# Kernel optimization log

Hardware: AMD Instinct MI355X
Metric: run time of the kernel (lower is better)

The kernel has to match this reference:

```python
import jax, jax.numpy as jnp
import numpy as np

# static architecture constants (match init_kwargs)
H, D, N_BASIS, MEM_LEN, QLEN = 16, 128, 1024, 512, 2048
RIDGE = 0.5
BASIS_SIGMAS = (0.005, 0.01)


def _gaussian_pdf(x, mu, sigma):
    return jnp.exp(-0.5 * ((x - mu) / sigma) ** 2) / (sigma * jnp.sqrt(2.0 * jnp.pi))


def _basis_params(n):
    # torch.meshgrid(linspace(0,1,n//2), sigmas, indexing='ij') then flatten
    m = jnp.linspace(0.0, 1.0, n // len(BASIS_SIGMAS)).astype(jnp.float32)
    mu = jnp.repeat(m, len(BASIS_SIGMAS))
    sigma = jnp.tile(jnp.asarray(BASIS_SIGMAS, jnp.float32), n // len(BASIS_SIGMAS))
    return mu, sigma


def _compute_G(l, b_mu, b_sigma, n):
    # padded linear positions on [-0.5+shift, 1.5-shift], l even -> 2l points
    shift = 1.0 / (2 * l)
    pos = jnp.linspace(-0.5 + shift, 1.5 - shift, 2 * l).astype(jnp.float32)
    F = _gaussian_pdf(pos[None, :], b_mu[:, None], b_sigma[:, None])  # [N, 2l]
    # G = F^T (F F^T + ridge I)^{-1}, then crop padding rows -> [l, N]
    G = jnp.linalg.solve(F @ F.T + RIDGE * jnp.eye(n, dtype=jnp.float32), F).T
    return G[l // 2: -(l // 2)]


def _forward(k, q, W_key, W_val, W_out, w_mu, w_sigma):
    d = H * D
    b_mu, b_sigma = _basis_params(N_BASIS)
    k = k[:, -512:, :]                                   # forward truncates memory
    l = k.shape[1]
    G = _compute_G(l, b_mu, b_sigma, N_BASIS)            # [l, N]
    # value_function: project signal onto basis coefficients B -> [1, N, d]
    B = jnp.einsum('bld,ln->bnd', k, G)
    keys = (B @ W_key.T).reshape(1, N_BASIS, H, D).transpose(0, 2, 1, 3)    # [1,H,N,D]
    values = (B @ W_val.T).reshape(1, N_BASIS, H, D).transpose(0, 2, 1, 3)  # [1,H,N,D]
    scores = jnp.einsum('bhqd,bhnd->bhqn', q / jnp.sqrt(jnp.float32(D)), keys)
    mu = jax.nn.sigmoid(scores @ w_mu)[..., None]                           # [1,H,Q,1]
    sigma_sq = jnp.maximum(jax.nn.softplus(scores @ w_sigma), 1e-4)[..., None]
    # continuous softmax over Gaussian RBFs: r_j = E_{t~N(mu,sigma_sq)}[psi_j(t)]
    # closed form: N(mu; b_mu_j, sigma_sq + b_sigma_j^2)
    r = _gaussian_pdf(b_mu, mu, jnp.sqrt(sigma_sq + b_sigma ** 2))          # [1,H,Q,N]
    context = jnp.einsum('bhqn,bhnd->bqhd', r, values).reshape(1, QLEN, d)
    return context @ W_out.T


def setup_inputs() -> dict:
    key = jax.random.key(0)
    ks = jax.random.split(key, 7)
    d = H * D
    s = 0.02
    return {
        'k': jax.random.normal(ks[0], (1, MEM_LEN, d), jnp.float32),
        'q': jax.random.normal(ks[1], (1, H, QLEN, D), jnp.float32),
        'W_key': jax.random.normal(ks[2], (d, d), jnp.float32) * s,
        'W_val': jax.random.normal(ks[3], (d, d), jnp.float32) * s,
        'W_out': jax.random.normal(ks[4], (d, d), jnp.float32) * s,
        'w_mu': jax.random.normal(ks[5], (N_BASIS,), jnp.float32) * s,
        'w_sigma': jax.random.normal(ks[6], (N_BASIS,), jnp.float32) * s,
        'new_doc': 1,
    }


def reference(k, q, W_key, W_val, W_out, w_mu, w_sigma, new_doc):
    # new_doc=True -> B_past/x_past reset, so only the fresh-memory path runs
    return _forward(k, q, W_key, W_val, W_out, w_mu, w_sigma)
```

## Files before the change

### kernel.cpp

```cpp
#include <hip/hip_runtime.h>
#include <hip/hip_bf16.h>
#include <vector>
#include <cmath>
#include <cstring>

using bf16 = __hip_bfloat16;
typedef short s16x8 __attribute__((ext_vector_type(8)));
typedef float f32x4 __attribute__((ext_vector_type(4)));

static constexpr int kH = 16, kD = 128, kNB = 1024, kML = 512, kQL = 2048, kDM = 2048;

static void compute_Gt_host(float* Gt) {
  const int n = kNB, P = 2 * kML;
  std::vector<double> F((size_t)n * P), A((size_t)n * n), pos(P);
  const double shift = 1.0 / (double)P;
  const double p0 = -0.5 + shift, p1 = 1.5 - shift;
  for (int i = 0; i < P; i++) pos[i] = p0 + (p1 - p0) * (double)i / (double)(P - 1);
  const double c0 = 0.3989422804014327;
  std::vector<int> lo(n), hi(n);
  for (int b = 0; b < n; b++) {
    double mu = (double)(b >> 1) / 511.0;
    double sg = (b & 1) ? 0.01 : 0.005;
    double c = c0 / sg;
    double* Fb = &F[(size_t)b * P];
    for (int i = 0; i < P; i++) { double t = (pos[i] - mu) / sg; Fb[i] = c * exp(-0.5 * t * t); }
    int l = 0; while (l < P - 1 && pos[l] < mu - 14.0 * sg) l++;
    int h = P - 1; while (h > 0 && pos[h] > mu + 14.0 * sg) h--;
    lo[b] = l; hi[b] = h;
  }
  for (int i = 0; i < n; i++) {
    const double* fi = &F[(size_t)i * P];
    for (int j = 0; j <= i; j++) {
      const double* fj = &F[(size_t)j * P];
      int a = lo[i] > lo[j] ? lo[i] : lo[j];
      int b2 = hi[i] < hi[j] ? hi[i] : hi[j];
      double s = 0.0;
      for (int k2 = a; k2 <= b2; k2++) s += fi[k2] * fj[k2];
      A[(size_t)i * n + j] = s;
      if (i != j) A[(size_t)j * n + i] = s;
    }
    A[(size_t)i * n + i] += 0.5;
  }
  for (int j = 0; j < n; j++) {
    double* Aj = &A[(size_t)j * n];
    double d = Aj[j];
    for (int k2 = 0; k2 < j; k2++) d -= Aj[k2] * Aj[k2];
    d = std::sqrt(d); Aj[j] = d;
    double inv = 1.0 / d;
    for (int i = j + 1; i < n; i++) {
      double* Ai = &A[(size_t)i * n];
      double s = Ai[j];
      for (int k2 = 0; k2 < j; k2++) s -= Ai[k2] * Aj[k2];
      Ai[j] = s * inv;
    }
  }
  for (int i = 0; i < n; i++) {
    double* yi = &F[(size_t)i * P];
    const double* Ai = &A[(size_t)i * n];
    for (int k2 = 0; k2 < i; k2++) {
      double lik = Ai[k2];
      const double* yk = &F[(size_t)k2 * P];
      for (int t = 0; t < P; t++) yi[t] -= lik * yk[t];
    }
    double inv = 1.0 / Ai[i];
    for (int t = 0; t < P; t++) yi[t] *= inv;
  }
  for (int i = n - 1; i >= 0; i--) {
    double* xi = &F[(size_t)i * P];
    for (int k2 = i + 1; k2 < n; k2++) {
      double lki = A[(size_t)k2 * n + i];
      const double* xk = &F[(size_t)k2 * P];
      for (int t = 0; t < P; t++) xi[t] -= lki * xk[t];
    }
    double inv = 1.0 / A[(size_t)i * n + i];
    for (int t = 0; t < P; t++) xi[t] *= inv;
  }
  for (int b = 0; b < n; b++)
    for (int l = 0; l < kML; l++)
      Gt[(size_t)b * kML + l] = (float)F[(size_t)b * P + (kML / 2) + l];
}

static unsigned short f2bf_host(float x) {
  unsigned u; std::memcpy(&u, &x, 4);
  unsigned r = (u + 0x7FFFu + ((u >> 16) & 1u)) >> 16;
  return (unsigned short)r;
}
static float bf2f_host(unsigned short b) {
  unsigned u = ((unsigned)b) << 16; float f; std::memcpy(&f, &u, 4); return f;
}

namespace {
struct Init {
  float* d_GtTf = nullptr;
  unsigned short* d_Gth = nullptr;
  unsigned short* d_Gtl = nullptr;
  float* h_GtTf_pinned = nullptr;
  unsigned short* h_Gth_pinned = nullptr;
  unsigned short* h_Gtl_pinned = nullptr;
  std::vector<float> h_GtTf;
  std::vector<unsigned short> h_Gth, h_Gtl;
  Init() {
    std::vector<float> h_Gt((size_t)kNB * kML);
    compute_Gt_host(h_Gt.data());
    h_GtTf.resize(h_Gt.size());
    h_Gth.resize(h_Gt.size());
    h_Gtl.resize(h_Gt.size());
    for (int n = 0; n < kNB; n++)
      for (int l = 0; l < kML; l++) {
        float v = h_Gt[(size_t)n * kML + l];
        h_GtTf[(size_t)l * kNB + n] = v;
        unsigned short hb = f2bf_host(v);
        h_Gth[(size_t)n * kML + l] = hb;
        h_Gtl[(size_t)n * kML + l] = f2bf_host(v - bf2f_host(hb));
      }
    const size_t fb = h_Gt.size() * 4, bb = h_Gt.size() * 2;
    if (hipMalloc((void**)&d_GtTf, fb) == hipSuccess) {
      if (hipMemcpy(d_GtTf, h_GtTf.data(), fb, hipMemcpyHostToDevice) != hipSuccess) { hipFree(d_GtTf); d_GtTf = nullptr; }
    }
    if (hipMalloc((void**)&d_Gth, bb) == hipSuccess) {
      if (hipMemcpy(d_Gth, h_Gth.data(), bb, hipMemcpyHostToDevice) != hipSuccess) { hipFree(d_Gth); d_Gth = nullptr; }
    }
    if (hipMalloc((void**)&d_Gtl, bb) == hipSuccess) {
      if (hipMemcpy(d_Gtl, h_Gtl.data(), bb, hipMemcpyHostToDevice) != hipSuccess) { hipFree(d_Gtl); d_Gtl = nullptr; }
    }
    if (!d_GtTf && hipHostMalloc((void**)&h_GtTf_pinned, fb, 0) == hipSuccess)
      std::memcpy(h_GtTf_pinned, h_GtTf.data(), fb);
    if (!d_Gth && hipHostMalloc((void**)&h_Gth_pinned, bb, 0) == hipSuccess)
      std::memcpy(h_Gth_pinned, h_Gth.data(), bb);
    if (!d_Gtl && hipHostMalloc((void**)&h_Gtl_pinned, bb, 0) == hipSuccess)
      std::memcpy(h_Gtl_pinned, h_Gtl.data(), bb);
  }
};
Init g_init;
}

__device__ inline short f2bf(float x) {
  unsigned u = __float_as_uint(x);
  unsigned r = (u + 0x7FFFu + ((u >> 16) & 1u)) >> 16;
  return (short)r;
}
__device__ inline float bf2f(short b) {
  return __uint_as_float(((unsigned)(unsigned short)b) << 16);
}

__device__ inline void gload16(const void* g, void* l) {
  __builtin_amdgcn_global_load_lds(
      (__attribute__((address_space(1))) void*)(g),
      (__attribute__((address_space(3))) void*)(l),
      16, 0, 0);
}

__global__ __launch_bounds__(256) void detect_kernel(const unsigned short* __restrict__ q,
                                                     int* __restrict__ flag) {
  int t = threadIdx.x;
  int bad = 0;
  for (int i = t; i < 4096; i += 256) {
    int e = (q[i] >> 7) & 0xFF;
    if (e >= 0x98) bad = 1;
  }
  __shared__ int s[256];
  s[t] = bad; __syncthreads();
  for (int k2 = 128; k2 > 0; k2 >>= 1) { if (t < k2) s[t] |= s[t + k2]; __syncthreads(); }
  if (t == 0) *flag = s[0];
}

__global__ __launch_bounds__(256) void conv_bf16(const void* __restrict__ in,
                                                 short* __restrict__ out, int n4,
                                                 const int* __restrict__ flag) {
  int i = blockIdx.x * 256 + threadIdx.x;
  if (i >= n4) return;
  if (*flag) {
    float4 v = ((const float4*)in)[i];
    short4 o; o.x = f2bf(v.x); o.y = f2bf(v.y); o.z = f2bf(v.z); o.w = f2bf(v.w);
    ((short4*)out)[i] = o;
  } else {
    ((short4*)out)[i] = ((const short4*)in)[i];
  }
}

__global__ __launch_bounds__(256) void gw_kernel(const float* __restrict__ GtT,
                                                 const void* __restrict__ wmu,
                                                 const void* __restrict__ wsg,
                                                 float* __restrict__ gw,
                                                 const int* __restrict__ flag) {
  const bool f32 = (*flag != 0);
  const int l = blockIdx.x, t = threadIdx.x;
  const float* row = GtT + (long long)l * kNB;
  float a = 0.f, b = 0.f;
  for (int n = t; n < kNB; n += 256) {
    float g = row[n];
    float wm_ = f32 ? ((const float*)wmu)[n] : bf2f(((const short*)wmu)[n]);
    float ws_ = f32 ? ((const float*)wsg)[n] : bf2f(((const short*)wsg)[n]);
    a += g * wm_; b += g * ws_;
  }
  __shared__ float red[2][256];
  red[0][t] = a; red[1][t] = b;
  __syncthreads();
  for (int s = 128; s > 0; s >>= 1) {
    if (t < s) { red[0][t] += red[0][t + s]; red[1][t] += red[1][t + s]; }
    __syncthreads();
  }
  if (t == 0) { gw[l] = red[0][0]; gw[kML + l] = red[1][0]; }
}

__global__ __launch_bounds__(256) void bwk_kernel(const void* __restrict__ kin,
                                                  const float* __restrict__ gw,
                                                  float* __restrict__ bw,
                                                  const int* __restrict__ flag) {
  const bool f32 = (*flag != 0);
  int j = blockIdx.x * 256 + threadIdx.x;
  int l0 = blockIdx.y * 32;
  float a = 0.f, b = 0.f;
  for (int l = l0; l < l0 + 32; l++) {
    float kv = f32 ? ((const float*)kin)[(long long)l * kDM + j]
                   : bf2f(((const short*)kin)[(long long)l * kDM + j]);
    a += kv * gw[l]; b += kv * gw[kML + l];
  }
  atomicAdd(&bw[j], a);
  atomicAdd(&bw[kDM + j], b);
}

__global__ __launch_bounds__(256) void kw_kernel(const void* __restrict__ Wk,
                                                 const float* __restrict__ bw,
                                                 float* __restrict__ kw,
                                                 const int* __restrict__ flag) {
  const bool f32 = (*flag != 0);
  int i = blockIdx.x;
  float smu = 0.f, ssg = 0.f;
  if (f32) {
    const float* row = (const float*)Wk + (long long)i * kDM;
    for (int j = threadIdx.x; j < kDM; j += 256) { float w = row[j]; smu += w * bw[j]; ssg += w * bw[kDM + j]; }
  } else {
    const short* row = (const short*)Wk + (long long)i * kDM;
    for (int j = threadIdx.x; j < kDM; j += 256) { float w = bf2f(row[j]); smu += w * bw[j]; ssg += w * bw[kDM + j]; }
  }
  __shared__ float red[2][256];
  red[0][threadIdx.x] = smu; red[1][threadIdx.x] = ssg;
  __syncthreads();
  for (int s = 128; s > 0; s >>= 1) {
    if (threadIdx.x < (unsigned)s) {
      red[0][threadIdx.x] += red[0][threadIdx.x + s];
      red[1][threadIdx.x] += red[1][threadIdx.x + s];
    }
    __syncthreads();
  }
  if (threadIdx.x == 0) { kw[i] = red[0][0]; kw[kDM + i] = red[1][0]; }
}

__global__ __launch_bounds__(256) void musig_kernel(const void* __restrict__ q,
                                                    const float* __restrict__ kw,
                                                    float* __restrict__ mu,
                                                    float* __restrict__ sigsq,
                                                    const int* __restrict__ flag) {
  const bool f32 = (*flag != 0);
  int w = threadIdx.x >> 6, lane = threadIdx.x & 63;
  int idx = blockIdx.x * 4 + w;
  int h = idx >> 11;
  const float* kmu = kw + h * kD;
  const float* ksg = kw + kDM + h * kD;
  float q0, q1;
  if (f32) {
    const float* qrow = (const float*)q + (long long)idx * kD;
    q0 = qrow[lane]; q1 = qrow[lane + 64];
  } else {
    const short* qrow = (const short*)q + (long long)idx * kD;
    q0 = bf2f(qrow[lane]); q1 = bf2f(qrow[lane + 64]);
  }
  float a = q0 * kmu[lane] + q1 * kmu[lane + 64];
  float b = q0 * ksg[lane] + q1 * ksg[lane + 64];
  for (int s = 32; s > 0; s >>= 1) { a += __shfl_xor(a, s); b += __shfl_xor(b, s); }
  if (lane == 0) {
    const float inv_sqrt_d = 0.08838834764831845f;
    float zm = a * inv_sqrt_d, zs = b * inv_sqrt_d;
    mu[idx] = 1.f / (1.f + __expf(-zm));
    float sp = (zs > 20.f) ? zs : log1pf(__expf(zs));
    sigsq[idx] = fmaxf(sp, 1e-4f);
  }
}

template <int CSTORE>
__global__ __launch_bounds__(256) void mfma_gemm_bt(
    const short* __restrict__ A0, int lda, long long sA,
    const short* __restrict__ BT0, int ldb, long long sB,
    void* __restrict__ C0, int ldc, long long sC,
    int K, const int* __restrict__ flag) {
  __shared__ s16x8 lA[512];
  __shared__ s16x8 lB[512];
  const short* A = A0 + (long long)blockIdx.z * sA;
  const short* BT = BT0 + (long long)blockIdx.z * sB;
  const int t = threadIdx.x;
  const int wave = t >> 6, lane = t & 63;
  const int quad = lane >> 4, l16 = lane & 15;
  const int wm = wave >> 1, wn = wave & 1;
  const int m0 = blockIdx.y * 128, n0 = blockIdx.x * 128;
  const int srow = lane & 15, skc = lane >> 4;
  f32x4 acc[4][4];
  const f32x4 z = {0.f, 0.f, 0.f, 0.f};
#pragma unroll
  for (int i = 0; i < 4; i++)
#pragma unroll
    for (int j = 0; j < 4; j++) acc[i][j] = z;
  for (int k0 = 0; k0 < K; k0 += 32) {
#pragma unroll
    for (int i = 0; i < 2; i++) {
      int sub = wave + i * 4;
      int m = sub * 16 + srow;
      gload16(A + (long long)(m0 + m) * lda + k0 + skc * 8, &lA[sub * 64]);
      gload16(BT + (long long)(n0 + m) * ldb + k0 + skc * 8, &lB[sub * 64]);
    }
    __syncthreads();
    s16x8 af[4], bfr[4];
#pragma unroll
    for (int i = 0; i < 4; i++) af[i] = lA[(wm * 4 + i) * 64 + lane];
#pragma unroll
    for (int j = 0; j < 4; j++) bfr[j] = lB[(wn * 4 + j) * 64 + lane];
#pragma unroll
    for (int i = 0; i < 4; i++)
#pragma unroll
      for (int j = 0; j < 4; j++)
        acc[i][j] = __builtin_amdgcn_mfma_f32_16x16x32_bf16(af[i], bfr[j], acc[i][j], 0, 0, 0);
    __syncthreads();
  }
  if (CSTORE == 0) {
    short* Cp = (short*)C0 + (long long)blockIdx.z * sC;
#pragma unroll
    for (int i = 0; i < 4; i++)
#pragma unroll
      for (int j = 0; j < 4; j++) {
        int gn = n0 + (wn * 4 + j) * 16 + l16;
#pragma unroll
        for (int rg = 0; rg < 4; rg++) {
          int gm = m0 + (wm * 4 + i) * 16 + quad * 4 + rg;
          Cp[(long long)gm * ldc + gn] = f2bf(acc[i][j][rg]);
        }
      }
  } else {
    if (*flag) {
      float* Cp = (float*)C0 + (long long)blockIdx.z * sC;
#pragma unroll
      for (int i = 0; i < 4; i++)
#pragma unroll
        for (int j = 0; j < 4; j++) {
          int gn = n0 + (wn * 4 + j) * 16 + l16;
#pragma unroll
          for (int rg = 0; rg < 4; rg++) {
            int gm = m0 + (wm * 4 + i) * 16 + quad * 4 + rg;
            Cp[(long long)gm * ldc + gn] = acc[i][j][rg];
          }
        }
    } else {
      short* Cp = (short*)C0 + (long long)blockIdx.z * sC;
#pragma unroll
      for (int i = 0; i < 4; i++)
#pragma unroll
        for (int j = 0; j < 4; j++) {
          int gn = n0 + (wn * 4 + j) * 16 + l16;
#pragma unroll
          for (int rg = 0; rg < 4; rg++) {
            int gm = m0 + (wm * 4 + i) * 16 + quad * 4 + rg;
            Cp[(long long)gm * ldc + gn] = f2bf(acc[i][j][rg]);
          }
        }
    }
  }
}

__global__ __launch_bounds__(256) void mfma_gemm_sk(
    const short* __restrict__ A0, int lda,
    const short* __restrict__ BT0, int ldb,
    float* __restrict__ P, int ldc) {
  __shared__ s16x8 lA[512], lB[512];
  const int t = threadIdx.x;
  const int wave = t >> 6, lane = t & 63;
  const int quad = lane >> 4, l16 = lane & 15;
  const int wm = wave >> 1, wn = wave & 1;
  const int m0 = blockIdx.y * 128, n0 = blockIdx.x * 128;
  const int kbeg = blockIdx.z * 512, kend = kbeg + 512;
  const int srow = lane & 15, skc = lane >> 4;
  f32x4 acc[4][4];
  const f32x4 z = {0.f, 0.f, 0.f, 0.f};
#pragma unroll
  for (int i = 0; i < 4; i++)
#pragma unroll
    for (int j = 0; j < 4; j++) acc[i][j] = z;
  for (int k0 = kbeg; k0 < kend; k0 += 32) {
#pragma unroll
    for (int i = 0; i < 2; i++) {
      int sub = wave + i * 4;
      int m = sub * 16 + srow;
      gload16(A0 + (long long)(m0 + m) * lda + k0 + skc * 8, &lA[sub * 64]);
      gload16(BT0 + (long long)(n0 + m) * ldb + k0 + skc * 8, &lB[sub * 64]);
    }
    __syncthreads();
    s16x8 af[4], bfr[4];
#pragma unroll
    for (int i = 0; i < 4; i++) af[i] = lA[(wm * 4 + i) * 64 + lane];
#pragma unroll
    for (int j = 0; j < 4; j++) bfr[j] = lB[(wn * 4 + j) * 64 + lane];
#pragma unroll
    for (int i = 0; i < 4; i++)
#pragma unroll
      for (int j = 0; j < 4; j++)
        acc[i][j] = __builtin_amdgcn_mfma_f32_16x16x32_bf16(af[i], bfr[j], acc[i][j], 0, 0, 0);
    __syncthreads();
  }
  float* Cp = P + (long long)blockIdx.z * kML * kDM;
#pragma unroll
  for (int i = 0; i < 4; i++)
#pragma unroll
    for (int j = 0; j < 4; j++) {
      int gn = n0 + (wn * 4 + j) * 16 + l16;
#pragma unroll
      for (int rg = 0; rg < 4; rg++) {
        int gm = m0 + (wm * 4 + i) * 16 + quad * 4 + rg;
        Cp[(long long)gm * ldc + gn] = acc[i][j][rg];
      }
    }
}

__global__ __launch_bounds__(256) void reduceT_kernel(const float* __restrict__ P,
                                                      short* __restrict__ kvT) {
  __shared__ float tile[64][65];
  const int bd = blockIdx.x, bl = blockIdx.y;
  const int tx = threadIdx.x & 63, ty = threadIdx.x >> 6;
  for (int i = ty; i < 64; i += 4) {
    int l = bl * 64 + i, d = bd * 64 + tx;
    float s = 0.f;
#pragma unroll
    for (int z = 0; z < 4; z++) s += P[((long long)z * kML + l) * kDM + d];
    tile[i][tx] = s;
  }
  __syncthreads();
  for (int i = ty; i < 64; i += 4) {
    int d = bd * 64 + i, l = bl * 64 + tx;
    kvT[(long long)d * kML + l] = f2bf(tile[tx][i]);
  }
}

__global__ __launch_bounds__(256) void mfma_gemm_bt2(
    const short* __restrict__ A0, int lda,
    const short* __restrict__ BTh, const short* __restrict__ BTl, int ldb,
    short* __restrict__ Ch, short* __restrict__ Cl, int ldc, int K) {
  __shared__ s16x8 lA[512], lBh[512], lBl[512];
  const int t = threadIdx.x;
  const int wave = t >> 6, lane = t & 63;
  const int quad = lane >> 4, l16 = lane & 15;
  const int wm = wave >> 1, wn = wave & 1;
  const int m0 = blockIdx.y * 128, n0 = blockIdx.x * 128;
  const int srow = lane & 15, skc = lane >> 4;
  f32x4 acc[4][4];
  const f32x4 z = {0.f, 0.f, 0.f, 0.f};
#pragma unroll
  for (int i = 0; i < 4; i++)
#pragma unroll
    for (int j = 0; j < 4; j++) acc[i][j] = z;
  for (int k0 = 0; k0 < K; k0 += 32) {
#pragma unroll
    for (int i = 0; i < 2; i++) {
      int sub = wave + i * 4;
      int m = sub * 16 + srow;
      gload16(A0 + (long long)(m0 + m) * lda + k0 + skc * 8, &lA[sub * 64]);
      gload16(BTh + (long long)(n0 + m) * ldb + k0 + skc * 8, &lBh[sub * 64]);
      gload16(BTl + (long long)(n0 + m) * ldb + k0 + skc * 8, &lBl[sub * 64]);
    }
    __syncthreads();
    s16x8 af[4], bh[4], bl[4];
#pragma unroll
    for (int i = 0; i < 4; i++) af[i] = lA[(wm * 4 + i) * 64 + lane];
#pragma unroll
    for (int j = 0; j < 4; j++) {
      bh[j] = lBh[(wn * 4 + j) * 64 + lane];
      bl[j] = lBl[(wn * 4 + j) * 64 + lane];
    }
#pragma unroll
    for (int i = 0; i < 4; i++)
#pragma unroll
      for (int j = 0; j < 4; j++) {
        acc[i][j] = __builtin_amdgcn_mfma_f32_16x16x32_bf16(af[i], bh[j], acc[i][j], 0, 0, 0);
        acc[i][j] = __builtin_amdgcn_mfma_f32_16x16x32_bf16(af[i], bl[j], acc[i][j], 0, 0, 0);
      }
    __syncthreads();
  }
#pragma unroll
  for (int i = 0; i < 4; i++)
#pragma unroll
    for (int j = 0; j < 4; j++) {
      int gn = n0 + (wn * 4 + j) * 16 + l16;
#pragma unroll
      for (int rg = 0; rg < 4; rg++) {
        int gm = m0 + (wm * 4 + i) * 16 + quad * 4 + rg;
        float v = acc[i][j][rg];
        short hb = f2bf(v);
        Ch[(long long)gm * ldc + gn] = hb;
        Cl[(long long)gm * ldc + gn] = f2bf(v - bf2f(hb));
      }
    }
}

__global__ __launch_bounds__(256) void mfma_rv(
    const float* __restrict__ mu_all, const float* __restrict__ s2_all,
    const short* __restrict__ VTh, const short* __restrict__ VTl,
    short* __restrict__ ctx) {
  __shared__ s16x8 lAh[512], lAl[512], lBh[512], lBl[512];
  const int t = threadIdx.x;
  const int wave = t >> 6, lane = t & 63;
  const int quad = lane >> 4, l16 = lane & 15;
  const int wm = wave >> 1, wn = wave & 1;
  const int h = blockIdx.z;
  const int m0 = blockIdx.y * 128;
  const int r0 = t >> 2, kc = t & 3;
  const int srow = lane & 15, skc = lane >> 4;
  const long long voff = (long long)h * kD * kNB;
  float muv[2], ivs[2][2], cof[2][2];
#pragma unroll
  for (int i = 0; i < 2; i++) {
    int row = h * kQL + m0 + r0 + i * 64;
    float m_ = mu_all[row], s2 = s2_all[row];
    ivs[i][0] = rsqrtf(s2 + 2.5e-5f);
    ivs[i][1] = rsqrtf(s2 + 1e-4f);
    cof[i][0] = 0.3989422804014327f * ivs[i][0];
    cof[i][1] = 0.3989422804014327f * ivs[i][1];
    muv[i] = m_;
  }
  f32x4 acc[4][4];
  const f32x4 z = {0.f, 0.f, 0.f, 0.f};
#pragma unroll
  for (int i = 0; i < 4; i++)
#pragma unroll
    for (int j = 0; j < 4; j++) acc[i][j] = z;
  for (int k0 = 0; k0 < kNB; k0 += 32) {
#pragma unroll
    for (int i = 0; i < 2; i++) {
      int sub = wave + i * 4;
      int m = sub * 16 + srow;
      gload16(VTh + voff + (long long)m * kNB + k0 + skc * 8, &lBh[sub * 64]);
      gload16(VTl + voff + (long long)m * kNB + k0 + skc * 8, &lBl[sub * 64]);
    }
#pragma unroll
    for (int i = 0; i < 2; i++) {
      int m = r0 + i * 64;
      int cidx = (m >> 4) * 64 + kc * 16 + (m & 15);
      s16x8 hv, lv;
#pragma unroll
      for (int jj = 0; jj < 8; jj++) {
        int n = k0 + kc * 8 + jj;
        float bmu = (float)(n >> 1) * (1.f / 511.f);
        int p = jj & 1;
        float tt = (bmu - muv[i]) * ivs[i][p];
        float v = cof[i][p] * __expf(-0.5f * tt * tt);
        short hb = f2bf(v);
        hv[jj] = hb;
        lv[jj] = f2bf(v - bf2f(hb));
      }
      lAh[cidx] = hv;
      lAl[cidx] = lv;
    }
    __syncthreads();
    s16x8 ah[4], al[4], bh[4], bl[4];
#pragma unroll
    for (int i = 0; i < 4; i++) {
      ah[i] = lAh[(wm * 4 + i) * 64 + lane];
      al[i] = lAl[(wm * 4 + i) * 64 + lane];
    }
#pragma unroll
    for (int j = 0; j < 4; j++) {
      bh[j] = lBh[(wn * 4 + j) * 64 + lane];
      bl[j] = lBl[(wn * 4 + j) * 64 + lane];
    }
#pragma unroll
    for (int i = 0; i < 4; i++)
#pragma unroll
      for (int j = 0; j < 4; j++) {
        acc[i][j] = __builtin_amdgcn_mfma_f32_16x16x32_bf16(ah[i], bh[j], acc[i][j], 0, 0, 0);
        acc[i][j] = __builtin_amdgcn_mfma_f32_16x16x32_bf16(ah[i], bl[j], acc[i][j], 0, 0, 0);
        acc[i][j] = __builtin_amdgcn_mfma_f32_16x16x32_bf16(al[i], bh[j], acc[i][j], 0, 0, 0);
      }
    __syncthreads();
  }
  short* Cp = ctx + h * kD;
#pragma unroll
  for (int i = 0; i < 4; i++)
#pragma unroll
    for (int j = 0; j < 4; j++) {
      int gn = (wn * 4 + j) * 16 + l16;
#pragma unroll
      for (int rg = 0; rg < 4; rg++) {
        int gm = m0 + (wm * 4 + i) * 16 + quad * 4 + rg;
        Cp[(long long)gm * kDM + gn] = f2bf(acc[i][j][rg]);
      }
    }
}

extern "C" void kernel_launch(void* const* d_in, const int* in_sizes, int n_in,
                              void* d_out, int out_size, void* d_ws, size_t ws_size,
                              hipStream_t stream) {
  (void)in_sizes; (void)n_in; (void)out_size; (void)ws_size;
  const void* kmem = d_in[0];
  const void* q    = d_in[1];
  const void* Wk   = d_in[2];
  const void* Wv   = d_in[3];
  const void* Wo   = d_in[4];
  const void* wmu  = d_in[5];
  const void* wsg  = d_in[6];

  char* ws = (char*)d_ws;
  short* k_bf  = (short*)ws;
  short* kvT   = (short*)(ws + ((size_t)2 << 20));
  short* Wv_bf = (short*)(ws + ((size_t)4 << 20));
  short* Wo_bf = Wv_bf;
  float* Pbuf  = (float*)(ws + ((size_t)12 << 20));
  short* VTh   = (short*)(ws + ((size_t)12 << 20));
  short* VTl   = (short*)(ws + ((size_t)16 << 20));
  short* ctx   = (short*)(ws + ((size_t)20 << 20));
  float* tail  = (float*)(ws + ((size_t)28 << 20));
  float* gw    = tail;
  float* bw    = gw + 2 * kML;
  float* kw    = bw + 2 * kDM;
  float* mu    = kw + 2 * kDM;
  float* sigsq = mu + kH * kQL;
  int*   flag  = (int*)(sigsq + kH * kQL);
  float* gtffall = (float*)(ws + ((size_t)28 << 20) + ((size_t)1 << 19));
  short* ghfall  = (short*)(ws + ((size_t)30 << 20) + ((size_t)1 << 19));
  short* glfall  = (short*)(ws + ((size_t)31 << 20) + ((size_t)1 << 19));

  const float* GtTf = g_init.d_GtTf;
  if (!GtTf) {
    const void* src = g_init.h_GtTf_pinned ? (const void*)g_init.h_GtTf_pinned
                                           : (const void*)g_init.h_GtTf.data();
    hipMemcpyAsync(gtffall, src, (size_t)kNB * kML * 4, hipMemcpyHostToDevice, stream);
    GtTf = gtffall;
  }
  const short* Gh = (const short*)g_init.d_Gth;
  if (!Gh) {
    const void* src = g_init.h_Gth_pinned ? (const void*)g_init.h_Gth_pinned
                                          : (const void*)g_init.h_Gth.data();
    hipMemcpyAsync(ghfall, src, (size_t)kNB * kML * 2, hipMemcpyHostToDevice, stream);
    Gh = ghfall;
  }
  const short* Gl = (const short*)g_init.d_Gtl;
  if (!Gl) {
    const void* src = g_init.h_Gtl_pinned ? (const void*)g_init.h_Gtl_pinned
                                          : (const void*)g_init.h_Gtl.data();
    hipMemcpyAsync(glfall, src, (size_t)kNB * kML * 2, hipMemcpyHostToDevice, stream);
    Gl = glfall;
  }

  detect_kernel<<<1, 256, 0, stream>>>((const unsigned short*)q, flag);

  conv_bf16<<<(kML * kDM / 4 + 255) / 256, 256, 0, stream>>>(kmem, k_bf, kML * kDM / 4, flag);
  conv_bf16<<<(kDM * kDM / 4 + 255) / 256, 256, 0, stream>>>(Wv, Wv_bf, kDM * kDM / 4, flag);

  gw_kernel<<<kML, 256, 0, stream>>>(GtTf, wmu, wsg, gw, flag);
  hipMemsetAsync(bw, 0, 2 * kDM * sizeof(float), stream);
  bwk_kernel<<<dim3(kDM / 256, kML / 32), 256, 0, stream>>>(kmem, gw, bw, flag);
  kw_kernel<<<kDM, 256, 0, stream>>>(Wk, bw, kw, flag);
  musig_kernel<<<kH * kQL / 4, 256, 0, stream>>>(q, kw, mu, sigsq, flag);

  mfma_gemm_sk<<<dim3(kDM / 128, kML / 128, 4), 256, 0, stream>>>(
      k_bf, kDM, Wv_bf, kDM, Pbuf, kDM);
  reduceT_kernel<<<dim3(kDM / 64, kML / 64), 256, 0, stream>>>(Pbuf, kvT);

  conv_bf16<<<(kDM * kDM / 4 + 255) / 256, 256, 0, stream>>>(Wo, Wo_bf, kDM * kDM / 4, flag);

  mfma_gemm_bt2<<<dim3(kNB / 128, kDM / 128, 1), 256, 0, stream>>>(
      kvT, kML, Gh, Gl, kML, VTh, VTl, kNB, kML);

  mfma_rv<<<dim3(1, kQL / 128, kH), 256, 0, stream>>>(mu, sigsq, VTh, VTl, ctx);

  mfma_gemm_bt<2><<<dim3(kDM / 128, kQL / 128, 1), 256, 0, stream>>>(
      ctx, kDM, 0, Wo_bf, kDM, 0, d_out, kDM, 0, kDM, flag);
}
```

Before: 308.2 us.

## Double-buffer LDS tiles in all MFMA GEMM kernels to overlap loads with compute

```diff
diff --git a/kernel.cpp b/kernel.cpp
--- a/kernel.cpp
+++ b/kernel.cpp
@@ -284,8 +284,8 @@
     const short* __restrict__ BT0, int ldb, long long sB,
     void* __restrict__ C0, int ldc, long long sC,
     int K, const int* __restrict__ flag) {
-  __shared__ s16x8 lA[512];
-  __shared__ s16x8 lB[512];
+  __shared__ s16x8 lA[2][512];
+  __shared__ s16x8 lB[2][512];
   const short* A = A0 + (long long)blockIdx.z * sA;
   const short* BT = BT0 + (long long)blockIdx.z * sB;
   const int t = threadIdx.x;
@@ -300,26 +300,38 @@
   for (int i = 0; i < 4; i++)
 #pragma unroll
     for (int j = 0; j < 4; j++) acc[i][j] = z;
+#pragma unroll
+  for (int i = 0; i < 2; i++) {
+    int sub = wave + i * 4;
+    int m = sub * 16 + srow;
+    gload16(A + (long long)(m0 + m) * lda + skc * 8, &lA[0][sub * 64]);
+    gload16(BT + (long long)(n0 + m) * ldb + skc * 8, &lB[0][sub * 64]);
+  }
+  __syncthreads();
+  int cur = 0;
   for (int k0 = 0; k0 < K; k0 += 32) {
-#pragma unroll
-    for (int i = 0; i < 2; i++) {
-      int sub = wave + i * 4;
-      int m = sub * 16 + srow;
-      gload16(A + (long long)(m0 + m) * lda + k0 + skc * 8, &lA[sub * 64]);
-      gload16(BT + (long long)(n0 + m) * ldb + k0 + skc * 8, &lB[sub * 64]);
-    }
-    __syncthreads();
+    if (k0 + 32 < K) {
+      int nxt = cur ^ 1, kk = k0 + 32;
+#pragma unroll
+      for (int i = 0; i < 2; i++) {
+        int sub = wave + i * 4;
+        int m = sub * 16 + srow;
+        gload16(A + (long long)(m0 + m) * lda + kk + skc * 8, &lA[nxt][sub * 64]);
+        gload16(BT + (long long)(n0 + m) * ldb + kk + skc * 8, &lB[nxt][sub * 64]);
+      }
+    }
     s16x8 af[4], bfr[4];
 #pragma unroll
-    for (int i = 0; i < 4; i++) af[i] = lA[(wm * 4 + i) * 64 + lane];
-#pragma unroll
-    for (int j = 0; j < 4; j++) bfr[j] = lB[(wn * 4 + j) * 64 + lane];
+    for (int i = 0; i < 4; i++) af[i] = lA[cur][(wm * 4 + i) * 64 + lane];
+#pragma unroll
+    for (int j = 0; j < 4; j++) bfr[j] = lB[cur][(wn * 4 + j) * 64 + lane];
 #pragma unroll
     for (int i = 0; i < 4; i++)
 #pragma unroll
       for (int j = 0; j < 4; j++)
         acc[i][j] = __builtin_amdgcn_mfma_f32_16x16x32_bf16(af[i], bfr[j], acc[i][j], 0, 0, 0);
     __syncthreads();
+    cur ^= 1;
   }
   if (CSTORE == 0) {
     short* Cp = (short*)C0 + (long long)blockIdx.z * sC;
@@ -369,7 +381,7 @@
     const short* __restrict__ A0, int lda,
     const short* __restrict__ BT0, int ldb,
     float* __restrict__ P, int ldc) {
-  __shared__ s16x8 lA[512], lB[512];
+  __shared__ s16x8 lA[2][512], lB[2][512];
   const int t = threadIdx.x;
   const int wave = t >> 6, lane = t & 63;
   const int quad = lane >> 4, l16 = lane & 15;
@@ -383,26 +395,38 @@
   for (int i = 0; i < 4; i++)
 #pragma unroll
     for (int j = 0; j < 4; j++) acc[i][j] = z;
+#pragma unroll
+  for (int i = 0; i < 2; i++) {
+    int sub = wave + i * 4;
+    int m = sub * 16 + srow;
+    gload16(A0 + (long long)(m0 + m) * lda + kbeg + skc * 8, &lA[0][sub * 64]);
+    gload16(BT0 + (long long)(n0 + m) * ldb + kbeg + skc * 8, &lB[0][sub * 64]);
+  }
+  __syncthreads();
+  int cur = 0;
   for (int k0 = kbeg; k0 < kend; k0 += 32) {
-#pragma unroll
-    for (int i = 0; i < 2; i++) {
-      int sub = wave + i * 4;
-      int m = sub * 16 + srow;
-      gload16(A0 + (long long)(m0 + m) * lda + k0 + skc * 8, &lA[sub * 64]);
-      gload16(BT0 + (long long)(n0 + m) * ldb + k0 + skc * 8, &lB[sub * 64]);
-    }
-    __syncthreads();
+    if (k0 + 32 < kend) {
+      int nxt = cur ^ 1, kk = k0 + 32;
+#pragma unroll
+      for (int i = 0; i < 2; i++) {
+        int sub = wave + i * 4;
+        int m = sub * 16 + srow;
+        gload16(A0 + (long long)(m0 + m) * lda + kk + skc * 8, &lA[nxt][sub * 64]);
+        gload16(BT0 + (long long)(n0 + m) * ldb + kk + skc * 8, &lB[nxt][sub * 64]);
+      }
+    }
     s16x8 af[4], bfr[4];
 #pragma unroll
-    for (int i = 0; i < 4; i++) af[i] = lA[(wm * 4 + i) * 64 + lane];
-#pragma unroll
-    for (int j = 0; j < 4; j++) bfr[j] = lB[(wn * 4 + j) * 64 + lane];
+    for (int i = 0; i < 4; i++) af[i] = lA[cur][(wm * 4 + i) * 64 + lane];
+#pragma unroll
+    for (int j = 0; j < 4; j++) bfr[j] = lB[cur][(wn * 4 + j) * 64 + lane];
 #pragma unroll
     for (int i = 0; i < 4; i++)
 #pragma unroll
       for (int j = 0; j < 4; j++)
         acc[i][j] = __builtin_amdgcn_mfma_f32_16x16x32_bf16(af[i], bfr[j], acc[i][j], 0, 0, 0);
     __syncthreads();
+    cur ^= 1;
   }
   float* Cp = P + (long long)blockIdx.z * kML * kDM;
 #pragma unroll
@@ -441,7 +465,7 @@
     const short* __restrict__ A0, int lda,
     const short* __restrict__ BTh, const short* __restrict__ BTl, int ldb,
     short* __restrict__ Ch, short* __restrict__ Cl, int ldc, int K) {
-  __shared__ s16x8 lA[512], lBh[512], lBl[512];
+  __shared__ s16x8 lA[2][512], lBh[2][512], lBl[2][512];
   const int t = threadIdx.x;
   const int wave = t >> 6, lane = t & 63;
   const int quad = lane >> 4, l16 = lane & 15;
@@ -454,23 +478,35 @@
   for (int i = 0; i < 4; i++)
 #pragma unroll
     for (int j = 0; j < 4; j++) acc[i][j] = z;
+#pragma unroll
+  for (int i = 0; i < 2; i++) {
+    int sub = wave + i * 4;
+    int m = sub * 16 + srow;
+    gload16(A0 + (long long)(m0 + m) * lda + skc * 8, &lA[0][sub * 64]);
+    gload16(BTh + (long long)(n0 + m) * ldb + skc * 8, &lBh[0][sub * 64]);
+    gload16(BTl + (long long)(n0 + m) * ldb + skc * 8, &lBl[0][sub * 64]);
+  }
+  __syncthreads();
+  int cur = 0;
   for (int k0 = 0; k0 < K; k0 += 32) {
-#pragma unroll
-    for (int i = 0; i < 2; i++) {
-      int sub = wave + i * 4;
-      int m = sub * 16 + srow;
-      gload16(A0 + (long long)(m0 + m) * lda + k0 + skc * 8, &lA[sub * 64]);
-      gload16(BTh + (long long)(n0 + m) * ldb + k0 + skc * 8, &lBh[sub * 64]);
-      gload16(BTl + (long long)(n0 + m) * ldb + k0 + skc * 8, &lBl[sub * 64]);
-    }
-    __syncthreads();
+    if (k0 + 32 < K) {
+      int nxt = cur ^ 1, kk = k0 + 32;
+#pragma unroll
+      for (int i = 0; i < 2; i++) {
+        int sub = wave + i * 4;
+        int m = sub * 16 + srow;
+        gload16(A0 + (long long)(m0 + m) * lda + kk + skc * 8, &lA[nxt][sub * 64]);
+        gload16(BTh + (long long)(n0 + m) * ldb + kk + skc * 8, &lBh[nxt][sub * 64]);
+        gload16(BTl + (long long)(n0 + m) * ldb + kk + skc * 8, &lBl[nxt][sub * 64]);
+      }
+    }
     s16x8 af[4], bh[4], bl[4];
 #pragma unroll
-    for (int i = 0; i < 4; i++) af[i] = lA[(wm * 4 + i) * 64 + lane];
+    for (int i = 0; i < 4; i++) af[i] = lA[cur][(wm * 4 + i) * 64 + lane];
 #pragma unroll
     for (int j = 0; j < 4; j++) {
-      bh[j] = lBh[(wn * 4 + j) * 64 + lane];
-      bl[j] = lBl[(wn * 4 + j) * 64 + lane];
+      bh[j] = lBh[cur][(wn * 4 + j) * 64 + lane];
+      bl[j] = lBl[cur][(wn * 4 + j) * 64 + lane];
     }
 #pragma unroll
     for (int i = 0; i < 4; i++)
@@ -480,6 +516,7 @@
         acc[i][j] = __builtin_amdgcn_mfma_f32_16x16x32_bf16(af[i], bl[j], acc[i][j], 0, 0, 0);
       }
     __syncthreads();
+    cur ^= 1;
   }
 #pragma unroll
   for (int i = 0; i < 4; i++)
@@ -501,7 +538,7 @@
     const float* __restrict__ mu_all, const float* __restrict__ s2_all,
     const short* __restrict__ VTh, const short* __restrict__ VTl,
     short* __restrict__ ctx) {
-  __shared__ s16x8 lAh[512], lAl[512], lBh[512], lBl[512];
+  __shared__ s16x8 lAh[2][512], lAl[2][512], lBh[2][512], lBl[2][512];
   const int t = threadIdx.x;
   const int wave = t >> 6, lane = t & 63;
   const int quad = lane >> 4, l16 = lane & 15;
@@ -522,20 +559,16 @@
     cof[i][1] = 0.3989422804014327f * ivs[i][1];
     muv[i] = m_;
   }
-  f32x4 acc[4][4];
-  const f32x4 z = {0.f, 0.f, 0.f, 0.f};
-#pragma unroll
-  for (int i = 0; i < 4; i++)
-#pragma unroll
-    for (int j = 0; j < 4; j++) acc[i][j] = z;
-  for (int k0 = 0; k0 < kNB; k0 += 32) {
+  auto stageB = [&](int b, int kk) {
 #pragma unroll
     for (int i = 0; i < 2; i++) {
       int sub = wave + i * 4;
       int m = sub * 16 + srow;
-      gload16(VTh + voff + (long long)m * kNB + k0 + skc * 8, &lBh[sub * 64]);
-      gload16(VTl + voff + (long long)m * kNB + k0 + skc * 8, &lBl[sub * 64]);
-    }
+      gload16(VTh + voff + (long long)m * kNB + kk + skc * 8, &lBh[b][sub * 64]);
+      gload16(VTl + voff + (long long)m * kNB + kk + skc * 8, &lBl[b][sub * 64]);
+    }
+  };
+  auto stageA = [&](int b, int kk) {
 #pragma unroll
     for (int i = 0; i < 2; i++) {
       int m = r0 + i * 64;
@@ -543,7 +576,7 @@
       s16x8 hv, lv;
 #pragma unroll
       for (int jj = 0; jj < 8; jj++) {
-        int n = k0 + kc * 8 + jj;
+        int n = kk + kc * 8 + jj;
         float bmu = (float)(n >> 1) * (1.f / 511.f);
         int p = jj & 1;
         float tt = (bmu - muv[i]) * ivs[i][p];
@@ -552,20 +585,35 @@
         hv[jj] = hb;
         lv[jj] = f2bf(v - bf2f(hb));
       }
-      lAh[cidx] = hv;
-      lAl[cidx] = lv;
-    }
-    __syncthreads();
+      lAh[b][cidx] = hv;
+      lAl[b][cidx] = lv;
+    }
+  };
+  f32x4 acc[4][4];
+  const f32x4 z = {0.f, 0.f, 0.f, 0.f};
+#pragma unroll
+  for (int i = 0; i < 4; i++)
+#pragma unroll
+    for (int j = 0; j < 4; j++) acc[i][j] = z;
+  stageB(0, 0);
+  stageA(0, 0);
+  __syncthreads();
+  int cur = 0;
+  for (int k0 = 0; k0 < kNB; k0 += 32) {
+    if (k0 + 32 < kNB) {
+      stageB(cur ^ 1, k0 + 32);
+      stageA(cur ^ 1, k0 + 32);
+    }
     s16x8 ah[4], al[4], bh[4], bl[4];
 #pragma unroll
     for (int i = 0; i < 4; i++) {
-      ah[i] = lAh[(wm * 4 + i) * 64 + lane];
-      al[i] = lAl[(wm * 4 + i) * 64 + lane];
+      ah[i] = lAh[cur][(wm * 4 + i) * 64 + lane];
+      al[i] = lAl[cur][(wm * 4 + i) * 64 + lane];
     }
 #pragma unroll
     for (int j = 0; j < 4; j++) {
-      bh[j] = lBh[(wn * 4 + j) * 64 + lane];
-      bl[j] = lBl[(wn * 4 + j) * 64 + lane];
+      bh[j] = lBh[cur][(wn * 4 + j) * 64 + lane];
+      bl[j] = lBl[cur][(wn * 4 + j) * 64 + lane];
     }
 #pragma unroll
     for (int i = 0; i < 4; i++)
@@ -576,6 +624,7 @@
         acc[i][j] = __builtin_amdgcn_mfma_f32_16x16x32_bf16(al[i], bh[j], acc[i][j], 0, 0, 0);
       }
     __syncthreads();
+    cur ^= 1;
   }
   short* Cp = ctx + h * kD;
 #pragma unroll
```

Result: faster. 295.7 us (-4.1%).
